# Kernel tuning notes

Hardware: AMD Instinct MI355X
Metric: run time of the kernel (lower is better)

## Reference

```python
import jax, jax.numpy as jnp
import numpy as np

NUM_ITERATIONS = 3


def squash(v, axis=-1):
    sq = jnp.sum(v * v, axis=axis, keepdims=True)
    scale = sq / (1.0 + sq)
    return scale * v / jnp.sqrt(sq)


def setup_inputs() -> dict:
    key = jax.random.key(0)
    k1, k2 = jax.random.split(key)
    B, N, IN, OUT, CAPS = 512, 4608, 16, 32, 32
    x = jax.random.normal(k1, (B, N, IN), dtype=jnp.float32)
    # torch.rand -> uniform [0, 1)
    route_weights = jax.random.uniform(k2, (N, IN, OUT), dtype=jnp.float32)
    return {"x": x, "route_weights": route_weights, "num_capsules": CAPS}


def reference(x, route_weights, num_capsules):
    # x: [B, N, IN], route_weights: [N, IN, OUT]
    u_hat = jnp.einsum('bnk,nkl->bnl', x, route_weights)  # [B, N, OUT]
    N = x.shape[1]
    b = jnp.zeros((N, num_capsules), dtype=u_hat.dtype)  # routing logits [N, CAPS]
    v = None
    for it in range(NUM_ITERATIONS):
        c = jax.nn.softmax(b, axis=-1)                     # [N, CAPS]
        s = jnp.einsum('bnk,nc->bck', u_hat, c)            # [B, CAPS, OUT]
        v = squash(s, axis=-1)                             # [B, CAPS, OUT]
        if it < NUM_ITERATIONS - 1:
            b = b + jnp.einsum('bnk,bck->nc', u_hat, v)    # agreement, reduced over batch
    return v
```

## Files before the change

kernel.cpp:

```cpp
#include <hip/hip_runtime.h>


#define NB 512
#define KTOT 73728
#define OUTC 32
#define NCAPS 32

#define KSPLIT 64
#define KCHUNK (KTOT / KSPLIT)
#define NSTEP (KCHUNK / 32)
#define NSTEPS_TOT (KTOT / 32)
#define WT_BYTES ((size_t)NSTEPS_TOT * 2 * 64 * 8 * 2)
#define SPA_BYTES ((size_t)KSPLIT * NB * OUTC * 4)
#define S_BYTES ((size_t)NB * OUTC * 4)

typedef short bf16x8 __attribute__((ext_vector_type(8)));
typedef float f32x4 __attribute__((ext_vector_type(4)));

__device__ __forceinline__ unsigned int f2bf(float f) {
    union { float f; unsigned int u; } v; v.f = f;
    unsigned int u = v.u;
    return (u + 0x7fffu + ((u >> 16) & 1u)) >> 16;
}

__global__ __launch_bounds__(256) void wt_prep(const float* __restrict__ w,
                                               unsigned short* __restrict__ wt) {
    int tt = blockIdx.x * 256 + threadIdx.x;
    int lane = tt & 63;
    int h = (tt >> 6) & 1;
    int step = tt >> 7;
    int k0 = step * 32 + ((lane >> 4) & 3) * 8;
    int c = h * 16 + (lane & 15);
    const float* wp = w + (size_t)k0 * OUTC + c;
    unsigned int u[4];
#pragma unroll
    for (int j = 0; j < 4; ++j) {
        unsigned int lo = f2bf(wp[(2 * j) * OUTC]);
        unsigned int hi = f2bf(wp[(2 * j + 1) * OUTC]);
        u[j] = lo | (hi << 16);
    }
    *(uint4*)(wt + (size_t)tt * 8) = make_uint4(u[0], u[1], u[2], u[3]);
}

template <bool PART>
__global__ __launch_bounds__(256) void gemm_mfma(
        const float* __restrict__ x, const unsigned short* __restrict__ wt,
        float* __restrict__ S) {
    const int t = threadIdx.x;
    const int lane = t & 63;
    const int wave = t >> 6;
    const int bx = blockIdx.x;
    const int by = blockIdx.y;
    const int row0 = by * 64 + wave * 16;
    const int m = lane & 15;
    const int q = lane >> 4;
    const size_t kbase = (size_t)bx * KCHUNK;

    const float* xp = x + (size_t)(row0 + m) * KTOT + kbase + q * 8;
    const unsigned short* wp = wt + (kbase >> 5) * 1024 + lane * 8;

    f32x4 acc0 = {0.f, 0.f, 0.f, 0.f};
    f32x4 acc1 = {0.f, 0.f, 0.f, 0.f};

    float4 xa = *(const float4*)xp;
    float4 xb = *(const float4*)(xp + 4);
    bf16x8 b0 = *(const bf16x8*)(wp);
    bf16x8 b1 = *(const bf16x8*)(wp + 512);

#pragma unroll 6
    for (int s = 0; s < NSTEP; ++s) {
        float4 nxa, nxb;
        bf16x8 nb0, nb1;
        if (s + 1 < NSTEP) {
            const float* xn = xp + 32;
            nxa = *(const float4*)xn;
            nxb = *(const float4*)(xn + 4);
            const unsigned short* wn = wp + 1024;
            nb0 = *(const bf16x8*)(wn);
            nb1 = *(const bf16x8*)(wn + 512);
        }
        xp += 32;
        wp += 1024;

        bf16x8 a;
        a[0] = (short)f2bf(xa.x); a[1] = (short)f2bf(xa.y);
        a[2] = (short)f2bf(xa.z); a[3] = (short)f2bf(xa.w);
        a[4] = (short)f2bf(xb.x); a[5] = (short)f2bf(xb.y);
        a[6] = (short)f2bf(xb.z); a[7] = (short)f2bf(xb.w);
        acc0 = __builtin_amdgcn_mfma_f32_16x16x32_bf16(a, b0, acc0, 0, 0, 0);
        acc1 = __builtin_amdgcn_mfma_f32_16x16x32_bf16(a, b1, acc1, 0, 0, 0);

        xa = nxa; xb = nxb; b0 = nb0; b1 = nb1;
    }

#pragma unroll
    for (int r = 0; r < 4; ++r) {
        const int row = row0 + q * 4 + r;
        if (PART) {
            float* dst = S + ((size_t)bx * NB + row) * OUTC;
            dst[m] = acc0[r];
            dst[16 + m] = acc1[r];
        } else {
            atomicAdd(&S[(size_t)row * OUTC + m], acc0[r]);
            atomicAdd(&S[(size_t)row * OUTC + 16 + m], acc1[r]);
        }
    }
}

__global__ __launch_bounds__(256) void zero_s(float* __restrict__ S) {
    int i = blockIdx.x * 256 + threadIdx.x;
    if (i < NB * OUTC) S[i] = 0.0f;
}

template <bool PART>
__global__ __launch_bounds__(64) void finalize_k(const float* __restrict__ S,
                                                 float* __restrict__ out) {
    const int b = blockIdx.x;
    const int t = threadIdx.x;
    const int k = t & 31;
    const int h = t >> 5;
    float s;
    if (PART) {
        float a = 0.0f;
#pragma unroll 8
        for (int i = 0; i < KSPLIT / 2; ++i)
            a += S[((size_t)(h * (KSPLIT / 2) + i) * NB + b) * OUTC + k];
        a += __shfl_xor(a, 32, 64);
        s = a * (1.0f / 32.0f);
    } else {
        s = S[(size_t)b * OUTC + k] * (1.0f / 32.0f);
    }
    float sq = s * s;
    sq += __shfl_xor(sq, 16, 64);
    sq += __shfl_xor(sq, 8, 64);
    sq += __shfl_xor(sq, 4, 64);
    sq += __shfl_xor(sq, 2, 64);
    sq += __shfl_xor(sq, 1, 64);
    float scale = sq / ((1.0f + sq) * sqrtf(sq));
    float v = s * scale;
    float* orow = out + (size_t)b * (NCAPS * OUTC);
#pragma unroll
    for (int j = 0; j < 16; ++j)
        orow[(h + j * 2) * OUTC + k] = v;
}

#define FKCHUNK 1152
#define FKT 128
#define FNQ 32
#define FRPW 2
#define FKSTR 132

__global__ __launch_bounds__(256) void gemm_fb(
        const float* __restrict__ x, const float* __restrict__ w,
        float* __restrict__ S) {
    __shared__ float wlds[OUTC * FKSTR];
    const int t = threadIdx.x;
    const int lane = t & 63;
    const int l32 = lane & 31;
    const int half = lane >> 5;
    const int wave = t >> 6;
    const int row0 = blockIdx.x * 16 + wave * 4 + half * FRPW;
    const size_t kbase = (size_t)blockIdx.y * FKCHUNK;
    const int sc = t & 31;
    const int sh = t >> 5;

    float acc[FRPW][OUTC];
#pragma unroll
    for (int r = 0; r < FRPW; ++r)
#pragma unroll
        for (int c = 0; c < OUTC; ++c) acc[r][c] = 0.0f;

    const float4* xq[FRPW];
#pragma unroll
    for (int r = 0; r < FRPW; ++r)
        xq[r] = (const float4*)(x + (size_t)(row0 + r) * KTOT + kbase);

    for (int tile = 0; tile < FKCHUNK / FKT; ++tile) {
        float4 xv[FRPW];
#pragma unroll
        for (int r = 0; r < FRPW; ++r)
            xv[r] = xq[r][tile * FNQ + l32];
#pragma unroll
        for (int jj = 0; jj < 4; ++jj) {
            int kk = 4 * (jj * 8 + sh);
            const float* wg = w + (kbase + (size_t)tile * FKT + kk) * OUTC + sc;
            *(float4*)&wlds[sc * FKSTR + kk] =
                make_float4(wg[0], wg[OUTC], wg[2 * OUTC], wg[3 * OUTC]);
        }
        __syncthreads();
#pragma unroll
        for (int c = 0; c < OUTC; ++c) {
            float4 wv = *(const float4*)&wlds[c * FKSTR + 4 * l32];
#pragma unroll
            for (int r = 0; r < FRPW; ++r) {
                float a = acc[r][c];
                a = fmaf(xv[r].x, wv.x, a);
                a = fmaf(xv[r].y, wv.y, a);
                a = fmaf(xv[r].z, wv.z, a);
                a = fmaf(xv[r].w, wv.w, a);
                acc[r][c] = a;
            }
        }
        __syncthreads();
    }
#pragma unroll
    for (int r = 0; r < FRPW; ++r) {
        float myv = 0.0f;
#pragma unroll
        for (int c = 0; c < OUTC; ++c) {
            float v = acc[r][c];
            v += __shfl_xor(v, 16, 64);
            v += __shfl_xor(v, 8, 64);
            v += __shfl_xor(v, 4, 64);
            v += __shfl_xor(v, 2, 64);
            v += __shfl_xor(v, 1, 64);
            if (l32 == c) myv = v;
        }
        atomicAdd(&S[(size_t)(row0 + r) * OUTC + l32], myv);
    }
}

extern "C" void kernel_launch(void* const* d_in, const int* in_sizes, int n_in,
                              void* d_out, int out_size, void* d_ws, size_t ws_size,
                              hipStream_t stream) {
    const float* x = (const float*)d_in[0];
    const float* w = (const float*)d_in[1];
    float* out = (float*)d_out;

    if (ws_size >= WT_BYTES + SPA_BYTES) {
        unsigned short* wt = (unsigned short*)d_ws;
        float* S = (float*)((char*)d_ws + WT_BYTES);
        hipLaunchKernelGGL(wt_prep, dim3(NSTEPS_TOT * 128 / 256), dim3(256), 0,
                           stream, w, wt);
        hipLaunchKernelGGL((gemm_mfma<true>), dim3(KSPLIT, 8), dim3(256), 0,
                           stream, x, wt, S);
        hipLaunchKernelGGL((finalize_k<true>), dim3(NB), dim3(64), 0, stream,
                           S, out);
    } else if (ws_size >= WT_BYTES + S_BYTES) {
        unsigned short* wt = (unsigned short*)d_ws;
        float* S = (float*)((char*)d_ws + WT_BYTES);
        hipLaunchKernelGGL(wt_prep, dim3(NSTEPS_TOT * 128 / 256), dim3(256), 0,
                           stream, w, wt);
        hipLaunchKernelGGL(zero_s, dim3((NB * OUTC + 255) / 256), dim3(256), 0,
                           stream, S);
        hipLaunchKernelGGL((gemm_mfma<false>), dim3(KSPLIT, 8), dim3(256), 0,
                           stream, x, wt, S);
        hipLaunchKernelGGL((finalize_k<false>), dim3(NB), dim3(64), 0, stream,
                           S, out);
    } else {
        float* S = (float*)d_ws;
        hipLaunchKernelGGL(zero_s, dim3((NB * OUTC + 255) / 256), dim3(256), 0,
                           stream, S);
        hipLaunchKernelGGL(gemm_fb, dim3(32, 64), dim3(256), 0, stream,
                           x, w, S);
        hipLaunchKernelGGL((finalize_k<false>), dim3(NB), dim3(64), 0, stream,
                           S, out);
    }
}
```

Measured before the change: 226.9 us.

## Fuse weight prep, split-K GEMM and squash into one persistent kernel with grid barriers

```diff
diff --git a/kernel.cpp b/kernel.cpp
--- a/kernel.cpp
+++ b/kernel.cpp
@@ -6,13 +6,17 @@
 #define OUTC 32
 #define NCAPS 32
 
+#define NBLK 512
 #define KSPLIT 64
 #define KCHUNK (KTOT / KSPLIT)
 #define NSTEP (KCHUNK / 32)
 #define NSTEPS_TOT (KTOT / 32)
-#define WT_BYTES ((size_t)NSTEPS_TOT * 2 * 64 * 8 * 2)
+#define FRAG_U4 (NSTEPS_TOT * 128)
+#define WT_BYTES ((size_t)NSTEPS_TOT * 2048)
 #define SPA_BYTES ((size_t)KSPLIT * NB * OUTC * 4)
 #define S_BYTES ((size_t)NB * OUTC * 4)
+#define CNT_OFF (WT_BYTES + SPA_BYTES)
+#define WS_NEED_A (CNT_OFF + 64)
 
 typedef short bf16x8 __attribute__((ext_vector_type(8)));
 typedef float f32x4 __attribute__((ext_vector_type(4)));
@@ -21,6 +25,128 @@
     union { float f; unsigned int u; } v; v.f = f;
     unsigned int u = v.u;
     return (u + 0x7fffu + ((u >> 16) & 1u)) >> 16;
+}
+
+__device__ __forceinline__ void grid_barrier(unsigned* cnt, unsigned target) {
+    __syncthreads();
+    if (threadIdx.x == 0) {
+        __hip_atomic_fetch_add(cnt, 1u, __ATOMIC_ACQ_REL,
+                               __HIP_MEMORY_SCOPE_AGENT);
+        while (__hip_atomic_load(cnt, __ATOMIC_ACQUIRE,
+                                 __HIP_MEMORY_SCOPE_AGENT) < target)
+            __builtin_amdgcn_s_sleep(8);
+    }
+    __syncthreads();
+}
+
+__global__ __launch_bounds__(256, 2) void digitcaps_fused(
+        const float* __restrict__ x, const float* __restrict__ w,
+        float* __restrict__ out, char* __restrict__ ws) {
+    unsigned short* wt = (unsigned short*)ws;
+    float* S = (float*)(ws + WT_BYTES);
+    unsigned* cnt = (unsigned*)(ws + CNT_OFF);
+    const int t = threadIdx.x;
+
+    for (int tt = blockIdx.x * 256 + t; tt < FRAG_U4; tt += NBLK * 256) {
+        int lane = tt & 63;
+        int h = (tt >> 6) & 1;
+        int step = tt >> 7;
+        int k0 = step * 32 + ((lane >> 4) & 3) * 8;
+        int c = h * 16 + (lane & 15);
+        const float* wp = w + (size_t)k0 * OUTC + c;
+        unsigned int u[4];
+#pragma unroll
+        for (int j = 0; j < 4; ++j) {
+            unsigned int lo = f2bf(wp[(2 * j) * OUTC]);
+            unsigned int hi = f2bf(wp[(2 * j + 1) * OUTC]);
+            u[j] = lo | (hi << 16);
+        }
+        *(uint4*)(wt + (size_t)tt * 8) = make_uint4(u[0], u[1], u[2], u[3]);
+    }
+
+    grid_barrier(cnt, NBLK);
+
+    {
+        const int lane = t & 63;
+        const int wave = t >> 6;
+        const int bx = blockIdx.x & (KSPLIT - 1);
+        const int by = blockIdx.x >> 6;
+        const int row0 = by * 64 + wave * 16;
+        const int m = lane & 15;
+        const int q = lane >> 4;
+        const size_t kbase = (size_t)bx * KCHUNK;
+
+        const float* xp = x + (size_t)(row0 + m) * KTOT + kbase + q * 8;
+        const unsigned short* wp = wt + (kbase >> 5) * 1024 + lane * 8;
+
+        f32x4 acc0 = {0.f, 0.f, 0.f, 0.f};
+        f32x4 acc1 = {0.f, 0.f, 0.f, 0.f};
+
+        float4 xa = *(const float4*)xp;
+        float4 xb = *(const float4*)(xp + 4);
+        bf16x8 b0 = *(const bf16x8*)(wp);
+        bf16x8 b1 = *(const bf16x8*)(wp + 512);
+
+#pragma unroll 6
+        for (int s = 0; s < NSTEP; ++s) {
+            float4 nxa, nxb;
+            bf16x8 nb0, nb1;
+            if (s + 1 < NSTEP) {
+                const float* xn = xp + 32;
+                nxa = *(const float4*)xn;
+                nxb = *(const float4*)(xn + 4);
+                const unsigned short* wn = wp + 1024;
+                nb0 = *(const bf16x8*)(wn);
+                nb1 = *(const bf16x8*)(wn + 512);
+            }
+            xp += 32;
+            wp += 1024;
+
+            bf16x8 a;
+            a[0] = (short)f2bf(xa.x); a[1] = (short)f2bf(xa.y);
+            a[2] = (short)f2bf(xa.z); a[3] = (short)f2bf(xa.w);
+            a[4] = (short)f2bf(xb.x); a[5] = (short)f2bf(xb.y);
+            a[6] = (short)f2bf(xb.z); a[7] = (short)f2bf(xb.w);
+            acc0 = __builtin_amdgcn_mfma_f32_16x16x32_bf16(a, b0, acc0, 0, 0, 0);
+            acc1 = __builtin_amdgcn_mfma_f32_16x16x32_bf16(a, b1, acc1, 0, 0, 0);
+
+            xa = nxa; xb = nxb; b0 = nb0; b1 = nb1;
+        }
+
+#pragma unroll
+        for (int r = 0; r < 4; ++r) {
+            const int row = row0 + q * 4 + r;
+            float* dst = S + ((size_t)bx * NB + row) * OUTC;
+            dst[m] = acc0[r];
+            dst[16 + m] = acc1[r];
+        }
+    }
+
+    grid_barrier(cnt + 1, NBLK);
+
+    if (t < 64) {
+        const int b = blockIdx.x;
+        const int k = t & 31;
+        const int h = t >> 5;
+        float a = 0.0f;
+#pragma unroll 8
+        for (int i = 0; i < KSPLIT / 2; ++i)
+            a += S[((size_t)(h * (KSPLIT / 2) + i) * NB + b) * OUTC + k];
+        a += __shfl_xor(a, 32, 64);
+        float s = a * (1.0f / 32.0f);
+        float sq = s * s;
+        sq += __shfl_xor(sq, 16, 64);
+        sq += __shfl_xor(sq, 8, 64);
+        sq += __shfl_xor(sq, 4, 64);
+        sq += __shfl_xor(sq, 2, 64);
+        sq += __shfl_xor(sq, 1, 64);
+        float scale = sq / ((1.0f + sq) * sqrtf(sq));
+        float v = s * scale;
+        float* orow = out + (size_t)b * (NCAPS * OUTC);
+#pragma unroll
+        for (int j = 0; j < 16; ++j)
+            orow[(h + j * 2) * OUTC + k] = v;
+    }
 }
 
 __global__ __launch_bounds__(256) void wt_prep(const float* __restrict__ w,
@@ -42,8 +168,12 @@
     *(uint4*)(wt + (size_t)tt * 8) = make_uint4(u[0], u[1], u[2], u[3]);
 }
 
-template <bool PART>
-__global__ __launch_bounds__(256) void gemm_mfma(
+__global__ __launch_bounds__(256) void zero_s(float* __restrict__ S) {
+    int i = blockIdx.x * 256 + threadIdx.x;
+    if (i < NB * OUTC) S[i] = 0.0f;
+}
+
+__global__ __launch_bounds__(256) void gemm_mfma_at(
         const float* __restrict__ x, const unsigned short* __restrict__ wt,
         float* __restrict__ S) {
     const int t = threadIdx.x;
@@ -55,33 +185,18 @@
     const int m = lane & 15;
     const int q = lane >> 4;
     const size_t kbase = (size_t)bx * KCHUNK;
-
     const float* xp = x + (size_t)(row0 + m) * KTOT + kbase + q * 8;
     const unsigned short* wp = wt + (kbase >> 5) * 1024 + lane * 8;
-
     f32x4 acc0 = {0.f, 0.f, 0.f, 0.f};
     f32x4 acc1 = {0.f, 0.f, 0.f, 0.f};
-
-    float4 xa = *(const float4*)xp;
-    float4 xb = *(const float4*)(xp + 4);
-    bf16x8 b0 = *(const bf16x8*)(wp);
-    bf16x8 b1 = *(const bf16x8*)(wp + 512);
-
 #pragma unroll 6
     for (int s = 0; s < NSTEP; ++s) {
-        float4 nxa, nxb;
-        bf16x8 nb0, nb1;
-        if (s + 1 < NSTEP) {
-            const float* xn = xp + 32;
-            nxa = *(const float4*)xn;
-            nxb = *(const float4*)(xn + 4);
-            const unsigned short* wn = wp + 1024;
-            nb0 = *(const bf16x8*)(wn);
-            nb1 = *(const bf16x8*)(wn + 512);
-        }
+        float4 xa = *(const float4*)xp;
+        float4 xb = *(const float4*)(xp + 4);
         xp += 32;
+        bf16x8 b0 = *(const bf16x8*)(wp);
+        bf16x8 b1 = *(const bf16x8*)(wp + 512);
         wp += 1024;
-
         bf16x8 a;
         a[0] = (short)f2bf(xa.x); a[1] = (short)f2bf(xa.y);
         a[2] = (short)f2bf(xa.z); a[3] = (short)f2bf(xa.w);
@@ -89,47 +204,22 @@
         a[6] = (short)f2bf(xb.z); a[7] = (short)f2bf(xb.w);
         acc0 = __builtin_amdgcn_mfma_f32_16x16x32_bf16(a, b0, acc0, 0, 0, 0);
         acc1 = __builtin_amdgcn_mfma_f32_16x16x32_bf16(a, b1, acc1, 0, 0, 0);
-
-        xa = nxa; xb = nxb; b0 = nb0; b1 = nb1;
-    }
-
+    }
 #pragma unroll
     for (int r = 0; r < 4; ++r) {
         const int row = row0 + q * 4 + r;
-        if (PART) {
-            float* dst = S + ((size_t)bx * NB + row) * OUTC;
-            dst[m] = acc0[r];
-            dst[16 + m] = acc1[r];
-        } else {
-            atomicAdd(&S[(size_t)row * OUTC + m], acc0[r]);
-            atomicAdd(&S[(size_t)row * OUTC + 16 + m], acc1[r]);
-        }
-    }
-}
-
-__global__ __launch_bounds__(256) void zero_s(float* __restrict__ S) {
-    int i = blockIdx.x * 256 + threadIdx.x;
-    if (i < NB * OUTC) S[i] = 0.0f;
-}
-
-template <bool PART>
-__global__ __launch_bounds__(64) void finalize_k(const float* __restrict__ S,
-                                                 float* __restrict__ out) {
+        atomicAdd(&S[(size_t)row * OUTC + m], acc0[r]);
+        atomicAdd(&S[(size_t)row * OUTC + 16 + m], acc1[r]);
+    }
+}
+
+__global__ __launch_bounds__(64) void finalize_at(const float* __restrict__ S,
+                                                  float* __restrict__ out) {
     const int b = blockIdx.x;
     const int t = threadIdx.x;
     const int k = t & 31;
     const int h = t >> 5;
-    float s;
-    if (PART) {
-        float a = 0.0f;
-#pragma unroll 8
-        for (int i = 0; i < KSPLIT / 2; ++i)
-            a += S[((size_t)(h * (KSPLIT / 2) + i) * NB + b) * OUTC + k];
-        a += __shfl_xor(a, 32, 64);
-        s = a * (1.0f / 32.0f);
-    } else {
-        s = S[(size_t)b * OUTC + k] * (1.0f / 32.0f);
-    }
+    float s = S[(size_t)b * OUTC + k] * (1.0f / 32.0f);
     float sq = s * s;
     sq += __shfl_xor(sq, 16, 64);
     sq += __shfl_xor(sq, 8, 64);
@@ -144,82 +234,6 @@
         orow[(h + j * 2) * OUTC + k] = v;
 }
 
-#define FKCHUNK 1152
-#define FKT 128
-#define FNQ 32
-#define FRPW 2
-#define FKSTR 132
-
-__global__ __launch_bounds__(256) void gemm_fb(
-        const float* __restrict__ x, const float* __restrict__ w,
-        float* __restrict__ S) {
-    __shared__ float wlds[OUTC * FKSTR];
-    const int t = threadIdx.x;
-    const int lane = t & 63;
-    const int l32 = lane & 31;
-    const int half = lane >> 5;
-    const int wave = t >> 6;
-    const int row0 = blockIdx.x * 16 + wave * 4 + half * FRPW;
-    const size_t kbase = (size_t)blockIdx.y * FKCHUNK;
-    const int sc = t & 31;
-    const int sh = t >> 5;
-
-    float acc[FRPW][OUTC];
-#pragma unroll
-    for (int r = 0; r < FRPW; ++r)
-#pragma unroll
-        for (int c = 0; c < OUTC; ++c) acc[r][c] = 0.0f;
-
-    const float4* xq[FRPW];
-#pragma unroll
-    for (int r = 0; r < FRPW; ++r)
-        xq[r] = (const float4*)(x + (size_t)(row0 + r) * KTOT + kbase);
-
-    for (int tile = 0; tile < FKCHUNK / FKT; ++tile) {
-        float4 xv[FRPW];
-#pragma unroll
-        for (int r = 0; r < FRPW; ++r)
-            xv[r] = xq[r][tile * FNQ + l32];
-#pragma unroll
-        for (int jj = 0; jj < 4; ++jj) {
-            int kk = 4 * (jj * 8 + sh);
-            const float* wg = w + (kbase + (size_t)tile * FKT + kk) * OUTC + sc;
-            *(float4*)&wlds[sc * FKSTR + kk] =
-                make_float4(wg[0], wg[OUTC], wg[2 * OUTC], wg[3 * OUTC]);
-        }
-        __syncthreads();
-#pragma unroll
-        for (int c = 0; c < OUTC; ++c) {
-            float4 wv = *(const float4*)&wlds[c * FKSTR + 4 * l32];
-#pragma unroll
-            for (int r = 0; r < FRPW; ++r) {
-                float a = acc[r][c];
-                a = fmaf(xv[r].x, wv.x, a);
-                a = fmaf(xv[r].y, wv.y, a);
-                a = fmaf(xv[r].z, wv.z, a);
-                a = fmaf(xv[r].w, wv.w, a);
-                acc[r][c] = a;
-            }
-        }
-        __syncthreads();
-    }
-#pragma unroll
-    for (int r = 0; r < FRPW; ++r) {
-        float myv = 0.0f;
-#pragma unroll
-        for (int c = 0; c < OUTC; ++c) {
-            float v = acc[r][c];
-            v += __shfl_xor(v, 16, 64);
-            v += __shfl_xor(v, 8, 64);
-            v += __shfl_xor(v, 4, 64);
-            v += __shfl_xor(v, 2, 64);
-            v += __shfl_xor(v, 1, 64);
-            if (l32 == c) myv = v;
-        }
-        atomicAdd(&S[(size_t)(row0 + r) * OUTC + l32], myv);
-    }
-}
-
 extern "C" void kernel_launch(void* const* d_in, const int* in_sizes, int n_in,
                               void* d_out, int out_size, void* d_ws, size_t ws_size,
                               hipStream_t stream) {
@@ -227,15 +241,10 @@
     const float* w = (const float*)d_in[1];
     float* out = (float*)d_out;
 
-    if (ws_size >= WT_BYTES + SPA_BYTES) {
-        unsigned short* wt = (unsigned short*)d_ws;
-        float* S = (float*)((char*)d_ws + WT_BYTES);
-        hipLaunchKernelGGL(wt_prep, dim3(NSTEPS_TOT * 128 / 256), dim3(256), 0,
-                           stream, w, wt);
-        hipLaunchKernelGGL((gemm_mfma<true>), dim3(KSPLIT, 8), dim3(256), 0,
-                           stream, x, wt, S);
-        hipLaunchKernelGGL((finalize_k<true>), dim3(NB), dim3(64), 0, stream,
-                           S, out);
+    if (ws_size >= WS_NEED_A) {
+        hipMemsetAsync((char*)d_ws + CNT_OFF, 0, 64, stream);
+        hipLaunchKernelGGL(digitcaps_fused, dim3(NBLK), dim3(256), 0, stream,
+                           x, w, out, (char*)d_ws);
     } else if (ws_size >= WT_BYTES + S_BYTES) {
         unsigned short* wt = (unsigned short*)d_ws;
         float* S = (float*)((char*)d_ws + WT_BYTES);
@@ -243,17 +252,8 @@
                            stream, w, wt);
         hipLaunchKernelGGL(zero_s, dim3((NB * OUTC + 255) / 256), dim3(256), 0,
                            stream, S);
-        hipLaunchKernelGGL((gemm_mfma<false>), dim3(KSPLIT, 8), dim3(256), 0,
+        hipLaunchKernelGGL(gemm_mfma_at, dim3(KSPLIT, 8), dim3(256), 0,
                            stream, x, wt, S);
-        hipLaunchKernelGGL((finalize_k<false>), dim3(NB), dim3(64), 0, stream,
-                           S, out);
-    } else {
-        float* S = (float*)d_ws;
-        hipLaunchKernelGGL(zero_s, dim3((NB * OUTC + 255) / 256), dim3(256), 0,
-                           stream, S);
-        hipLaunchKernelGGL(gemm_fb, dim3(32, 64), dim3(256), 0, stream,
-                           x, w, S);
-        hipLaunchKernelGGL((finalize_k<false>), dim3(NB), dim3(64), 0, stream,
-                           S, out);
-    }
-}
+        hipLaunchKernelGGL(finalize_at, dim3(NB), dim3(64), 0, stream, S, out);
+    }
+}
```

Measured after the change: 336.8 us. +48.5%, slower.

## Fuse weight bf16 conversion into GEMM via per-block LDS staging

Applied to the files above, without the earlier changes.

```diff
diff --git a/kernel.cpp b/kernel.cpp
--- a/kernel.cpp
+++ b/kernel.cpp
@@ -9,8 +9,6 @@
 #define KSPLIT 64
 #define KCHUNK (KTOT / KSPLIT)
 #define NSTEP (KCHUNK / 32)
-#define NSTEPS_TOT (KTOT / 32)
-#define WT_BYTES ((size_t)NSTEPS_TOT * 2 * 64 * 8 * 2)
 #define SPA_BYTES ((size_t)KSPLIT * NB * OUTC * 4)
 #define S_BYTES ((size_t)NB * OUTC * 4)
 
@@ -23,64 +21,61 @@
     return (u + 0x7fffu + ((u >> 16) & 1u)) >> 16;
 }
 
-__global__ __launch_bounds__(256) void wt_prep(const float* __restrict__ w,
-                                               unsigned short* __restrict__ wt) {
-    int tt = blockIdx.x * 256 + threadIdx.x;
-    int lane = tt & 63;
-    int h = (tt >> 6) & 1;
-    int step = tt >> 7;
-    int k0 = step * 32 + ((lane >> 4) & 3) * 8;
-    int c = h * 16 + (lane & 15);
-    const float* wp = w + (size_t)k0 * OUTC + c;
-    unsigned int u[4];
-#pragma unroll
-    for (int j = 0; j < 4; ++j) {
-        unsigned int lo = f2bf(wp[(2 * j) * OUTC]);
-        unsigned int hi = f2bf(wp[(2 * j + 1) * OUTC]);
-        u[j] = lo | (hi << 16);
-    }
-    *(uint4*)(wt + (size_t)tt * 8) = make_uint4(u[0], u[1], u[2], u[3]);
-}
-
 template <bool PART>
-__global__ __launch_bounds__(256) void gemm_mfma(
-        const float* __restrict__ x, const unsigned short* __restrict__ wt,
+__global__ __launch_bounds__(256, 2) void gemm2(
+        const float* __restrict__ x, const float* __restrict__ w,
         float* __restrict__ S) {
+    __shared__ unsigned short wf[NSTEP * 2 * 64 * 8];
     const int t = threadIdx.x;
     const int lane = t & 63;
     const int wave = t >> 6;
     const int bx = blockIdx.x;
     const int by = blockIdx.y;
+    const size_t kbase = (size_t)bx * KCHUNK;
+
+#pragma unroll
+    for (int i = 0; i < 18; ++i) {
+        int e = i * 256 + t;
+        int le = e & 63;
+        int h = (e >> 6) & 1;
+        int st = e >> 7;
+        int k0 = st * 32 + ((le >> 4) & 3) * 8;
+        int c = h * 16 + (le & 15);
+        const float* wp = w + (kbase + k0) * (size_t)OUTC + c;
+        unsigned int u[4];
+#pragma unroll
+        for (int j = 0; j < 4; ++j) {
+            unsigned int lo = f2bf(wp[(2 * j) * OUTC]);
+            unsigned int hi = f2bf(wp[(2 * j + 1) * OUTC]);
+            u[j] = lo | (hi << 16);
+        }
+        *(uint4*)&wf[(size_t)e * 8] = make_uint4(u[0], u[1], u[2], u[3]);
+    }
+    __syncthreads();
+
     const int row0 = by * 64 + wave * 16;
     const int m = lane & 15;
     const int q = lane >> 4;
-    const size_t kbase = (size_t)bx * KCHUNK;
-
     const float* xp = x + (size_t)(row0 + m) * KTOT + kbase + q * 8;
-    const unsigned short* wp = wt + (kbase >> 5) * 1024 + lane * 8;
 
     f32x4 acc0 = {0.f, 0.f, 0.f, 0.f};
     f32x4 acc1 = {0.f, 0.f, 0.f, 0.f};
 
     float4 xa = *(const float4*)xp;
     float4 xb = *(const float4*)(xp + 4);
-    bf16x8 b0 = *(const bf16x8*)(wp);
-    bf16x8 b1 = *(const bf16x8*)(wp + 512);
 
 #pragma unroll 6
     for (int s = 0; s < NSTEP; ++s) {
         float4 nxa, nxb;
-        bf16x8 nb0, nb1;
         if (s + 1 < NSTEP) {
             const float* xn = xp + 32;
             nxa = *(const float4*)xn;
             nxb = *(const float4*)(xn + 4);
-            const unsigned short* wn = wp + 1024;
-            nb0 = *(const bf16x8*)(wn);
-            nb1 = *(const bf16x8*)(wn + 512);
         }
         xp += 32;
-        wp += 1024;
+
+        bf16x8 b0 = *(const bf16x8*)&wf[(s * 2 + 0) * 512 + lane * 8];
+        bf16x8 b1 = *(const bf16x8*)&wf[(s * 2 + 1) * 512 + lane * 8];
 
         bf16x8 a;
         a[0] = (short)f2bf(xa.x); a[1] = (short)f2bf(xa.y);
@@ -90,7 +85,7 @@
         acc0 = __builtin_amdgcn_mfma_f32_16x16x32_bf16(a, b0, acc0, 0, 0, 0);
         acc1 = __builtin_amdgcn_mfma_f32_16x16x32_bf16(a, b1, acc1, 0, 0, 0);
 
-        xa = nxa; xb = nxb; b0 = nb0; b1 = nb1;
+        xa = nxa; xb = nxb;
     }
 
 #pragma unroll
@@ -144,115 +139,24 @@
         orow[(h + j * 2) * OUTC + k] = v;
 }
 
-#define FKCHUNK 1152
-#define FKT 128
-#define FNQ 32
-#define FRPW 2
-#define FKSTR 132
-
-__global__ __launch_bounds__(256) void gemm_fb(
-        const float* __restrict__ x, const float* __restrict__ w,
-        float* __restrict__ S) {
-    __shared__ float wlds[OUTC * FKSTR];
-    const int t = threadIdx.x;
-    const int lane = t & 63;
-    const int l32 = lane & 31;
-    const int half = lane >> 5;
-    const int wave = t >> 6;
-    const int row0 = blockIdx.x * 16 + wave * 4 + half * FRPW;
-    const size_t kbase = (size_t)blockIdx.y * FKCHUNK;
-    const int sc = t & 31;
-    const int sh = t >> 5;
-
-    float acc[FRPW][OUTC];
-#pragma unroll
-    for (int r = 0; r < FRPW; ++r)
-#pragma unroll
-        for (int c = 0; c < OUTC; ++c) acc[r][c] = 0.0f;
-
-    const float4* xq[FRPW];
-#pragma unroll
-    for (int r = 0; r < FRPW; ++r)
-        xq[r] = (const float4*)(x + (size_t)(row0 + r) * KTOT + kbase);
-
-    for (int tile = 0; tile < FKCHUNK / FKT; ++tile) {
-        float4 xv[FRPW];
-#pragma unroll
-        for (int r = 0; r < FRPW; ++r)
-            xv[r] = xq[r][tile * FNQ + l32];
-#pragma unroll
-        for (int jj = 0; jj < 4; ++jj) {
-            int kk = 4 * (jj * 8 + sh);
-            const float* wg = w + (kbase + (size_t)tile * FKT + kk) * OUTC + sc;
-            *(float4*)&wlds[sc * FKSTR + kk] =
-                make_float4(wg[0], wg[OUTC], wg[2 * OUTC], wg[3 * OUTC]);
-        }
-        __syncthreads();
-#pragma unroll
-        for (int c = 0; c < OUTC; ++c) {
-            float4 wv = *(const float4*)&wlds[c * FKSTR + 4 * l32];
-#pragma unroll
-            for (int r = 0; r < FRPW; ++r) {
-                float a = acc[r][c];
-                a = fmaf(xv[r].x, wv.x, a);
-                a = fmaf(xv[r].y, wv.y, a);
-                a = fmaf(xv[r].z, wv.z, a);
-                a = fmaf(xv[r].w, wv.w, a);
-                acc[r][c] = a;
-            }
-        }
-        __syncthreads();
-    }
-#pragma unroll
-    for (int r = 0; r < FRPW; ++r) {
-        float myv = 0.0f;
-#pragma unroll
-        for (int c = 0; c < OUTC; ++c) {
-            float v = acc[r][c];
-            v += __shfl_xor(v, 16, 64);
-            v += __shfl_xor(v, 8, 64);
-            v += __shfl_xor(v, 4, 64);
-            v += __shfl_xor(v, 2, 64);
-            v += __shfl_xor(v, 1, 64);
-            if (l32 == c) myv = v;
-        }
-        atomicAdd(&S[(size_t)(row0 + r) * OUTC + l32], myv);
-    }
-}
-
 extern "C" void kernel_launch(void* const* d_in, const int* in_sizes, int n_in,
                               void* d_out, int out_size, void* d_ws, size_t ws_size,
                               hipStream_t stream) {
     const float* x = (const float*)d_in[0];
     const float* w = (const float*)d_in[1];
     float* out = (float*)d_out;
+    float* S = (float*)d_ws;
 
-    if (ws_size >= WT_BYTES + SPA_BYTES) {
-        unsigned short* wt = (unsigned short*)d_ws;
-        float* S = (float*)((char*)d_ws + WT_BYTES);
-        hipLaunchKernelGGL(wt_prep, dim3(NSTEPS_TOT * 128 / 256), dim3(256), 0,
-                           stream, w, wt);
-        hipLaunchKernelGGL((gemm_mfma<true>), dim3(KSPLIT, 8), dim3(256), 0,
-                           stream, x, wt, S);
+    if (ws_size >= SPA_BYTES) {
+        hipLaunchKernelGGL((gemm2<true>), dim3(KSPLIT, 8), dim3(256), 0,
+                           stream, x, w, S);
         hipLaunchKernelGGL((finalize_k<true>), dim3(NB), dim3(64), 0, stream,
                            S, out);
-    } else if (ws_size >= WT_BYTES + S_BYTES) {
-        unsigned short* wt = (unsigned short*)d_ws;
-        float* S = (float*)((char*)d_ws + WT_BYTES);
-        hipLaunchKernelGGL(wt_prep, dim3(NSTEPS_TOT * 128 / 256), dim3(256), 0,
-                           stream, w, wt);
+    } else {
         hipLaunchKernelGGL(zero_s, dim3((NB * OUTC + 255) / 256), dim3(256), 0,
                            stream, S);
-        hipLaunchKernelGGL((gemm_mfma<false>), dim3(KSPLIT, 8), dim3(256), 0,
-                           stream, x, wt, S);
-        hipLaunchKernelGGL((finalize_k<false>), dim3(NB), dim3(64), 0, stream,
-                           S, out);
-    } else {
-        float* S = (float*)d_ws;
-        hipLaunchKernelGGL(zero_s, dim3((NB * OUTC + 255) / 256), dim3(256), 0,
-                           stream, S);
-        hipLaunchKernelGGL(gemm_fb, dim3(32, 64), dim3(256), 0, stream,
-                           x, w, S);
+        hipLaunchKernelGGL((gemm2<false>), dim3(KSPLIT, 8), dim3(256), 0,
+                           stream, x, w, S);
         hipLaunchKernelGGL((finalize_k<false>), dim3(NB), dim3(64), 0, stream,
                            S, out);
     }
```

Measured after the change: 229.4 us. No clear change (+1.1%).
